# Kernel optimization log

Hardware: AMD Instinct MI355X
Metric: run time of the kernel (lower is better)

Reference implementation:

```python
import jax, jax.numpy as jnp
import numpy as np

N_VARS = 4096      # number of discrete variables
CARD = 16          # uniform cardinality per variable
N_HIDDEN = 256
POP = 1024         # pop_size (batch)
N_VISIBLE = N_VARS * CARD  # 65536


def setup_inputs() -> dict:
    key = jax.random.key(0)
    k1, k2, k3 = jax.random.split(key, 3)
    # hidden units are binary stochastic in the RBM; uniform [0,1) works for the math
    hidden = jax.random.uniform(k1, (POP, N_HIDDEN), dtype=jnp.float32)
    W = jax.random.normal(k2, (N_VISIBLE, N_HIDDEN), dtype=jnp.float32) * 0.01
    a = jax.random.normal(k3, (N_VISIBLE,), dtype=jnp.float32) * 0.01
    return {"hidden": hidden, "W": W, "a": a}


def reference(hidden, W, a):
    # prob_visible_given_hidden: activation = hidden @ W^T + a  -> [POP, N_VISIBLE]
    act = jnp.einsum('bh,vh->bv', hidden, W) + a
    # per-variable segmented softmax over each block of CARD visible units
    # (uniform cardinality -> reshape to [POP, N_VARS, CARD] and softmax on last axis)
    prob = jax.nn.softmax(act.reshape(POP, N_VARS, CARD), axis=-1)
    return prob.reshape(POP, N_VISIBLE)
```

## Files before the change

kernel.cpp:

```cpp
#include <hip/hip_runtime.h>
#include <hip/hip_bf16.h>


typedef short  bf16x8 __attribute__((ext_vector_type(8)));
typedef float  f32x4  __attribute__((ext_vector_type(4)));

#define NH    256
#define POP   1024
#define NVIS  65536
#define BM    128
#define BN    128
#define BK    32

__device__ __forceinline__ unsigned pack2bf(float lo, float hi) {
  return (__float_as_uint(hi) & 0xffff0000u) | (__float_as_uint(lo) >> 16);
}

__global__ __launch_bounds__(256) void rbm_softmax_kernel(
    const float* __restrict__ Wg,
    const float* __restrict__ Hg,
    const float* __restrict__ Ag,
    float* __restrict__ out)
{
  __shared__ short sA[BM * BK];
  __shared__ short sB[BN * BK];

  const int tid  = threadIdx.x;
  const int lane = tid & 63;
  const int wave = tid >> 6;
  const int wm   = wave & 1;
  const int wn   = wave >> 1;
  const int quad = lane >> 4;
  const int col  = lane & 15;

  const int m_base = blockIdx.y * BM;
  const int n_base = blockIdx.x * BN;

  const int r0  = tid >> 3;
  const int c0  = (tid & 7) * 4;

  f32x4 acc[4][4];
  #pragma unroll
  for (int i = 0; i < 4; ++i)
    #pragma unroll
    for (int j = 0; j < 4; ++j)
      acc[i][j] = f32x4{0.f, 0.f, 0.f, 0.f};

  for (int kk = 0; kk < NH / BK; ++kk) {
    const int k0 = kk * BK;
    if (kk) __syncthreads();

    const float* pa = Wg + (size_t)(m_base + r0) * NH + k0 + c0;
    const float* pb = Hg + (size_t)(n_base + r0) * NH + k0 + c0;
    #pragma unroll
    for (int i = 0; i < 4; ++i) {
      const float4 fa = *(const float4*)(pa + (size_t)i * 32 * NH);
      const float4 fb = *(const float4*)(pb + (size_t)i * 32 * NH);
      uint2 ua, ub;
      ua.x = pack2bf(fa.x, fa.y); ua.y = pack2bf(fa.z, fa.w);
      ub.x = pack2bf(fb.x, fb.y); ub.y = pack2bf(fb.z, fb.w);
      *(uint2*)&sA[(i * 32 + r0) * BK + c0] = ua;
      *(uint2*)&sB[(i * 32 + r0) * BK + c0] = ub;
    }
    __syncthreads();

    bf16x8 af[4], bfr[4];
    #pragma unroll
    for (int mt = 0; mt < 4; ++mt)
      af[mt] = *(const bf16x8*)&sA[(wm * 64 + mt * 16 + col) * BK + quad * 8];
    #pragma unroll
    for (int nt = 0; nt < 4; ++nt)
      bfr[nt] = *(const bf16x8*)&sB[(wn * 64 + nt * 16 + col) * BK + quad * 8];

    #pragma unroll
    for (int mt = 0; mt < 4; ++mt)
      #pragma unroll
      for (int nt = 0; nt < 4; ++nt)
        acc[mt][nt] = __builtin_amdgcn_mfma_f32_16x16x32_bf16(
            af[mt], bfr[nt], acc[mt][nt], 0, 0, 0);
  }

  #pragma unroll
  for (int mt = 0; mt < 4; ++mt) {
    const int v0 = m_base + wm * 64 + mt * 16 + quad * 4;
    const float4 av = *(const float4*)(Ag + v0);
    #pragma unroll
    for (int nt = 0; nt < 4; ++nt) {
      const int b = n_base + wn * 64 + nt * 16 + col;
      f32x4 c = acc[mt][nt];
      float x0 = c[0] + av.x, x1 = c[1] + av.y;
      float x2 = c[2] + av.z, x3 = c[3] + av.w;
      float mx = fmaxf(fmaxf(x0, x1), fmaxf(x2, x3));
      mx = fmaxf(mx, __shfl_xor(mx, 16));
      mx = fmaxf(mx, __shfl_xor(mx, 32));
      float e0 = __expf(x0 - mx), e1 = __expf(x1 - mx);
      float e2 = __expf(x2 - mx), e3 = __expf(x3 - mx);
      float s = (e0 + e1) + (e2 + e3);
      s += __shfl_xor(s, 16);
      s += __shfl_xor(s, 32);
      const float inv = 1.0f / s;
      float4 o;
      o.x = e0 * inv; o.y = e1 * inv; o.z = e2 * inv; o.w = e3 * inv;
      *(float4*)(out + (size_t)b * NVIS + v0) = o;
    }
  }
}

extern "C" void kernel_launch(void* const* d_in, const int* in_sizes, int n_in,
                              void* d_out, int out_size, void* d_ws, size_t ws_size,
                              hipStream_t stream) {
  const float* hidden = (const float*)d_in[0];
  const float* W      = (const float*)d_in[1];
  const float* a      = (const float*)d_in[2];
  float* out          = (float*)d_out;

  dim3 grid(POP / BN, NVIS / BM);
  rbm_softmax_kernel<<<grid, 256, 0, stream>>>(W, hidden, a, out);
}
```

Before: 429.1 us.

## Pre-convert W and hidden to bf16, load tiles via global_load_lds

Adds separate conversion kernels that write bf16 copies of W and hidden into the workspace. The GEMM then fills LDS directly with 16-byte global_load_lds transfers, which halves operand bytes per tile and removes the in-loop conversion. The softmax output is written with nontemporal stores. The cost is an extra pass over W (read fp32, write bf16) plus two more launches, and the original fused kernel is kept as a fallback when the workspace is too small.

```diff
diff --git a/kernel.cpp b/kernel.cpp
--- a/kernel.cpp
+++ b/kernel.cpp
@@ -12,13 +12,33 @@
 #define BN    128
 #define BK    32
 
+__device__ __forceinline__ void gld16(void* lds, const void* g) {
+  __builtin_amdgcn_global_load_lds(
+      (const __attribute__((address_space(1))) void*)g,
+      (__attribute__((address_space(3))) void*)lds,
+      16, 0, 0);
+}
 __device__ __forceinline__ unsigned pack2bf(float lo, float hi) {
   return (__float_as_uint(hi) & 0xffff0000u) | (__float_as_uint(lo) >> 16);
 }
 
-__global__ __launch_bounds__(256) void rbm_softmax_kernel(
-    const float* __restrict__ Wg,
-    const float* __restrict__ Hg,
+__global__ __launch_bounds__(256) void cvt_bf16_kernel(
+    const float* __restrict__ src, unsigned short* __restrict__ dst, int n8) {
+  int i = blockIdx.x * blockDim.x + threadIdx.x;
+  const int stride = gridDim.x * blockDim.x;
+  for (; i < n8; i += stride) {
+    const float4 f0 = ((const float4*)src)[2 * i];
+    const float4 f1 = ((const float4*)src)[2 * i + 1];
+    uint4 o;
+    o.x = pack2bf(f0.x, f0.y); o.y = pack2bf(f0.z, f0.w);
+    o.z = pack2bf(f1.x, f1.y); o.w = pack2bf(f1.z, f1.w);
+    ((uint4*)dst)[i] = o;
+  }
+}
+
+__global__ __launch_bounds__(256) void rbm_gemm_kernel(
+    const unsigned short* __restrict__ Wb,
+    const unsigned short* __restrict__ Hb,
     const float* __restrict__ Ag,
     float* __restrict__ out)
 {
@@ -36,9 +56,6 @@
   const int m_base = blockIdx.y * BM;
   const int n_base = blockIdx.x * BN;
 
-  const int r0  = tid >> 3;
-  const int c0  = (tid & 7) * 4;
-
   f32x4 acc[4][4];
   #pragma unroll
   for (int i = 0; i < 4; ++i)
@@ -50,17 +67,13 @@
     const int k0 = kk * BK;
     if (kk) __syncthreads();
 
-    const float* pa = Wg + (size_t)(m_base + r0) * NH + k0 + c0;
-    const float* pb = Hg + (size_t)(n_base + r0) * NH + k0 + c0;
-    #pragma unroll
-    for (int i = 0; i < 4; ++i) {
-      const float4 fa = *(const float4*)(pa + (size_t)i * 32 * NH);
-      const float4 fb = *(const float4*)(pb + (size_t)i * 32 * NH);
-      uint2 ua, ub;
-      ua.x = pack2bf(fa.x, fa.y); ua.y = pack2bf(fa.z, fa.w);
-      ub.x = pack2bf(fb.x, fb.y); ub.y = pack2bf(fb.z, fb.w);
-      *(uint2*)&sA[(i * 32 + r0) * BK + c0] = ua;
-      *(uint2*)&sB[(i * 32 + r0) * BK + c0] = ub;
+    #pragma unroll
+    for (int t = 0; t < 2; ++t) {
+      const int c   = t * 256 + tid;
+      const int row = c >> 2;
+      const int cio = (c & 3) * 8;
+      gld16(&sA[row * BK + cio], Wb + (size_t)(m_base + row) * NH + k0 + cio);
+      gld16(&sB[row * BK + cio], Hb + (size_t)(n_base + row) * NH + k0 + cio);
     }
     __syncthreads();
 
@@ -99,6 +112,76 @@
       s += __shfl_xor(s, 16);
       s += __shfl_xor(s, 32);
       const float inv = 1.0f / s;
+      f32x4 o;
+      o[0] = e0 * inv; o[1] = e1 * inv; o[2] = e2 * inv; o[3] = e3 * inv;
+      __builtin_nontemporal_store(o, (f32x4*)(out + (size_t)b * NVIS + v0));
+    }
+  }
+}
+
+__global__ __launch_bounds__(256) void rbm_softmax_fb(
+    const float* __restrict__ Wg, const float* __restrict__ Hg,
+    const float* __restrict__ Ag, float* __restrict__ out)
+{
+  __shared__ short sA[BM * BK];
+  __shared__ short sB[BN * BK];
+  const int tid = threadIdx.x, lane = tid & 63, wave = tid >> 6;
+  const int wm = wave & 1, wn = wave >> 1, quad = lane >> 4, col = lane & 15;
+  const int m_base = blockIdx.y * BM, n_base = blockIdx.x * BN;
+  const int r0 = tid >> 3, c0 = (tid & 7) * 4;
+  f32x4 acc[4][4];
+  #pragma unroll
+  for (int i = 0; i < 4; ++i)
+    #pragma unroll
+    for (int j = 0; j < 4; ++j) acc[i][j] = f32x4{0.f, 0.f, 0.f, 0.f};
+  for (int kk = 0; kk < NH / BK; ++kk) {
+    const int k0 = kk * BK;
+    if (kk) __syncthreads();
+    const float* pa = Wg + (size_t)(m_base + r0) * NH + k0 + c0;
+    const float* pb = Hg + (size_t)(n_base + r0) * NH + k0 + c0;
+    #pragma unroll
+    for (int i = 0; i < 4; ++i) {
+      const float4 fa = *(const float4*)(pa + (size_t)i * 32 * NH);
+      const float4 fb = *(const float4*)(pb + (size_t)i * 32 * NH);
+      uint2 ua, ub;
+      ua.x = pack2bf(fa.x, fa.y); ua.y = pack2bf(fa.z, fa.w);
+      ub.x = pack2bf(fb.x, fb.y); ub.y = pack2bf(fb.z, fb.w);
+      *(uint2*)&sA[(i * 32 + r0) * BK + c0] = ua;
+      *(uint2*)&sB[(i * 32 + r0) * BK + c0] = ub;
+    }
+    __syncthreads();
+    bf16x8 af[4], bfr[4];
+    #pragma unroll
+    for (int mt = 0; mt < 4; ++mt)
+      af[mt] = *(const bf16x8*)&sA[(wm * 64 + mt * 16 + col) * BK + quad * 8];
+    #pragma unroll
+    for (int nt = 0; nt < 4; ++nt)
+      bfr[nt] = *(const bf16x8*)&sB[(wn * 64 + nt * 16 + col) * BK + quad * 8];
+    #pragma unroll
+    for (int mt = 0; mt < 4; ++mt)
+      #pragma unroll
+      for (int nt = 0; nt < 4; ++nt)
+        acc[mt][nt] = __builtin_amdgcn_mfma_f32_16x16x32_bf16(
+            af[mt], bfr[nt], acc[mt][nt], 0, 0, 0);
+  }
+  #pragma unroll
+  for (int mt = 0; mt < 4; ++mt) {
+    const int v0 = m_base + wm * 64 + mt * 16 + quad * 4;
+    const float4 av = *(const float4*)(Ag + v0);
+    #pragma unroll
+    for (int nt = 0; nt < 4; ++nt) {
+      const int b = n_base + wn * 64 + nt * 16 + col;
+      f32x4 c = acc[mt][nt];
+      float x0 = c[0] + av.x, x1 = c[1] + av.y;
+      float x2 = c[2] + av.z, x3 = c[3] + av.w;
+      float mx = fmaxf(fmaxf(x0, x1), fmaxf(x2, x3));
+      mx = fmaxf(mx, __shfl_xor(mx, 16));
+      mx = fmaxf(mx, __shfl_xor(mx, 32));
+      float e0 = __expf(x0 - mx), e1 = __expf(x1 - mx);
+      float e2 = __expf(x2 - mx), e3 = __expf(x3 - mx);
+      float s = (e0 + e1) + (e2 + e3);
+      s += __shfl_xor(s, 16); s += __shfl_xor(s, 32);
+      const float inv = 1.0f / s;
       float4 o;
       o.x = e0 * inv; o.y = e1 * inv; o.z = e2 * inv; o.w = e3 * inv;
       *(float4*)(out + (size_t)b * NVIS + v0) = o;
@@ -114,6 +197,19 @@
   const float* a      = (const float*)d_in[2];
   float* out          = (float*)d_out;
 
+  const size_t w_elems = (size_t)NVIS * NH;
+  const size_t h_elems = (size_t)POP * NH;
+  const size_t need = (w_elems + h_elems) * sizeof(unsigned short);
+
   dim3 grid(POP / BN, NVIS / BM);
-  rbm_softmax_kernel<<<grid, 256, 0, stream>>>(W, hidden, a, out);
-}
+
+  if (ws_size >= need) {
+    unsigned short* Wb = (unsigned short*)d_ws;
+    unsigned short* Hb = Wb + w_elems;
+    cvt_bf16_kernel<<<2048, 256, 0, stream>>>(W, Wb, (int)(w_elems / 8));
+    cvt_bf16_kernel<<<128, 256, 0, stream>>>(hidden, Hb, (int)(h_elems / 8));
+    rbm_gemm_kernel<<<grid, 256, 0, stream>>>(Wb, Hb, a, out);
+  } else {
+    rbm_softmax_fb<<<grid, 256, 0, stream>>>(W, hidden, a, out);
+  }
+}
```

Result: faster. 394.5 us (-8.1%).
